# Optimization experiments

Measured on AMD Instinct MI355X. Metric: run time of the kernel, lower is better.

The kernel has to match this reference:

```python
import math
import jax, jax.numpy as jnp
from jax import lax
import numpy as np

N_IMG = 2
C = 128
IMG_H, IMG_W = 512, 1024
STRIDES = (4, 8, 16, 32, 64)
SIZES = (32.0, 64.0, 128.0, 256.0, 512.0)
RATIOS = (0.5, 1.0, 2.0)
A = len(RATIOS)
PRE_NMS_TOPK = 2000    # pre_nms_topk[self.training] with training=True
POST_NMS_TOPK = 1000   # post_nms_topk[self.training]
NMS_THRESH = 0.7
BATCH_PER_IMG = 256
POS_FRAC = 0.5
MIN_BOX_SIZE = 0.0
SCALE_CLAMP = math.log(1000.0 / 16.0)
MATCH_LOW, MATCH_HIGH = 0.3, 0.7


def cell_anchors(size):
    rs = jnp.asarray(RATIOS, jnp.float32)
    area = size * size
    w = jnp.sqrt(area / rs)
    h = w * rs
    return jnp.stack([-w / 2, -h / 2, w / 2, h / 2], axis=1)  # [A,4]


def level_anchors(H, W, stride, size):
    ca = cell_anchors(size)
    sx = jnp.arange(W, dtype=jnp.float32) * stride
    sy = jnp.arange(H, dtype=jnp.float32) * stride
    yy, xx = jnp.meshgrid(sy, sx, indexing="ij")
    shifts = jnp.stack([xx, yy, xx, yy], axis=-1).reshape(-1, 4)  # [H*W,4]
    return (shifts[:, None, :] + ca[None, :, :]).reshape(-1, 4)  # [H*W*A,4]


def pairwise_iou(a, b):
    lt = jnp.maximum(a[:, None, :2], b[None, :, :2])
    rb = jnp.minimum(a[:, None, 2:], b[None, :, 2:])
    wh = jnp.clip(rb - lt, 0.0)
    inter = wh[..., 0] * wh[..., 1]
    area_a = (a[:, 2] - a[:, 0]) * (a[:, 3] - a[:, 1])
    area_b = (b[:, 2] - b[:, 0]) * (b[:, 3] - b[:, 1])
    union = area_a[:, None] + area_b[None, :] - inter
    return jnp.where(inter > 0, inter / union, 0.0)


def get_deltas(src, tgt):
    sw = src[..., 2] - src[..., 0]; sh = src[..., 3] - src[..., 1]
    scx = src[..., 0] + 0.5 * sw;   scy = src[..., 1] + 0.5 * sh
    tw = tgt[..., 2] - tgt[..., 0]; th = tgt[..., 3] - tgt[..., 1]
    tcx = tgt[..., 0] + 0.5 * tw;   tcy = tgt[..., 1] + 0.5 * th
    return jnp.stack([(tcx - scx) / sw, (tcy - scy) / sh,
                      jnp.log(tw / sw), jnp.log(th / sh)], axis=-1)


def apply_deltas(deltas, boxes):
    w = boxes[..., 2] - boxes[..., 0]; h = boxes[..., 3] - boxes[..., 1]
    cx = boxes[..., 0] + 0.5 * w;      cy = boxes[..., 1] + 0.5 * h
    dx, dy = deltas[..., 0], deltas[..., 1]
    dw = jnp.minimum(deltas[..., 2], SCALE_CLAMP)
    dh = jnp.minimum(deltas[..., 3], SCALE_CLAMP)
    pcx = dx * w + cx; pcy = dy * h + cy
    pw = jnp.exp(dw) * w; ph = jnp.exp(dh) * h
    return jnp.stack([pcx - 0.5 * pw, pcy - 0.5 * ph,
                      pcx + 0.5 * pw, pcy + 0.5 * ph], axis=-1)


def conv(x, w, b):
    y = lax.conv_general_dilated(x, w, (1, 1), "SAME",
                                 dimension_numbers=("NCHW", "OIHW", "NCHW"))
    return y + b[None, :, None, None]


def rpn_forward_flat(feats, conv_w, conv_b, obj_w, obj_b, delta_w, delta_b):
    anchors, logits, deltas = [], [], []
    for (stride, size), f in zip(zip(STRIDES, SIZES), feats):
        N, _, H, W = f.shape
        h = jax.nn.relu(conv(f, conv_w, conv_b))
        lg = conv(h, obj_w, obj_b)       # [N,A,H,W]
        dl = conv(h, delta_w, delta_b)   # [N,4A,H,W]
        logits.append(lg.transpose(0, 2, 3, 1).reshape(N, -1))                     # [N,HWA]
        deltas.append(dl.reshape(N, A, 4, H, W).transpose(0, 3, 4, 1, 2).reshape(N, -1, 4))
        anchors.append(level_anchors(H, W, stride, size))
    return anchors, logits, deltas


def label_and_sample(gt_b, key, anchors_all):
    iou = pairwise_iou(gt_b, anchors_all)                 # [G,R]
    matched_idxs = jnp.argmax(iou, axis=0)
    matched_vals = jnp.max(iou, axis=0)
    labels = jnp.where(matched_vals >= MATCH_HIGH, 1,
             jnp.where(matched_vals >= MATCH_LOW, -1, 0))
    highest = jnp.max(iou, axis=1)                        # per-gt best IoU
    lq = jnp.any((iou == highest[:, None]) & (highest[:, None] > 0), axis=0)
    labels = jnp.where(lq, 1, labels)                     # allow_low_quality_matches
    R = labels.shape[0]
    kf, kb = jax.random.split(key)
    fg = labels == 1; bg = labels == 0
    num_fg = jnp.minimum(fg.sum(), int(POS_FRAC * BATCH_PER_IMG))
    num_bg = jnp.minimum(bg.sum(), BATCH_PER_IMG - num_fg)
    def pick(mask, k, num):
        pri = jnp.where(mask, jax.random.uniform(k, (R,)), jnp.inf)
        rank = jnp.argsort(jnp.argsort(pri))
        return rank < num
    sel_fg = pick(fg, kf, num_fg)
    sel_bg = pick(bg, kb, num_bg)
    labels = jnp.where(sel_fg, 1, jnp.where(sel_bg, 0, -1))
    return labels, gt_b[matched_idxs]


def losses_fn(anchors_all, logits_cat, deltas_cat, gt_labels, matched_gt):
    fg = (gt_labels == 1).astype(logits_cat.dtype)          # [N,R]
    gt_deltas = get_deltas(anchors_all[None], matched_gt)   # [N,R,4]
    loc = jnp.sum(jnp.abs(deltas_cat - gt_deltas) * fg[..., None])  # smooth_l1, beta=0
    valid = (gt_labels >= 0).astype(logits_cat.dtype)
    x = logits_cat
    bce = jnp.maximum(x, 0.0) - x * fg + jnp.log1p(jnp.exp(-jnp.abs(x)))
    cls = jnp.sum(bce * valid)
    norm = float(BATCH_PER_IMG) * logits_cat.shape[0]
    return jnp.stack([cls / norm, loc / norm])


def nms_keep(boxes, valid):
    # boxes are sorted by descending score; greedy suppression.
    K = boxes.shape[0]
    iou = pairwise_iou(boxes, boxes)
    idx = jnp.arange(K)
    def body(i, keep):
        sup = (iou[i] > NMS_THRESH) & (idx > i) & keep[i]
        return keep & ~sup
    return lax.fori_loop(0, K, body, valid)


def predict_proposals(anchors, logits, deltas):
    lvl_boxes, lvl_scores = [], []
    for anc, lg, dl in zip(anchors, logits, deltas):
        boxes = apply_deltas(dl, anc[None])             # [N,R_l,4]
        k = min(PRE_NMS_TOPK, lg.shape[1])
        ts, ti = lax.top_k(lg, k)                       # [N,k]
        tb = jnp.take_along_axis(boxes, ti[..., None], axis=1)
        tb = jnp.stack([jnp.clip(tb[..., 0], 0.0, IMG_W), jnp.clip(tb[..., 1], 0.0, IMG_H),
                        jnp.clip(tb[..., 2], 0.0, IMG_W), jnp.clip(tb[..., 3], 0.0, IMG_H)], -1)
        valid = ((tb[..., 2] - tb[..., 0]) > MIN_BOX_SIZE) & ((tb[..., 3] - tb[..., 1]) > MIN_BOX_SIZE)
        keep = jax.vmap(nms_keep)(tb, valid)
        lvl_boxes.append(tb)
        lvl_scores.append(jnp.where(keep, ts, -jnp.inf))
    all_b = jnp.concatenate(lvl_boxes, axis=1)
    all_s = jnp.concatenate(lvl_scores, axis=1)
    fs, fi = lax.top_k(all_s, POST_NMS_TOPK)
    fb = jnp.take_along_axis(all_b, fi[..., None], axis=1)
    return fb, fs


def setup_inputs() -> dict:
    key = jax.random.key(0)
    ks = jax.random.split(key, 12)
    out = {}
    for i, s in enumerate(STRIDES):
        out[f"feat_p{i+2}"] = jax.random.normal(ks[i], (N_IMG, C, IMG_H // s, IMG_W // s), jnp.float32)
    G = 32
    wh_scale = jnp.asarray([IMG_W, IMG_H], jnp.float32)
    cxy = jax.random.uniform(ks[5], (N_IMG, G, 2)) * wh_scale
    wh = 32.0 + jax.random.uniform(ks[6], (N_IMG, G, 2)) * 224.0
    x1y1 = jnp.clip(cxy - wh / 2, 0.0)
    x2y2 = jnp.maximum(jnp.minimum(cxy + wh / 2, wh_scale), x1y1 + 1.0)
    out["gt_boxes"] = jnp.concatenate([x1y1, x2y2], axis=-1)
    out["conv_w"] = 0.01 * jax.random.normal(ks[7], (C, C, 3, 3), jnp.float32)
    out["conv_b"] = jnp.zeros((C,), jnp.float32)
    out["obj_w"] = 0.01 * jax.random.normal(ks[8], (A, C, 1, 1), jnp.float32)
    out["obj_b"] = jnp.zeros((A,), jnp.float32)
    out["delta_w"] = 0.01 * jax.random.normal(ks[9], (4 * A, C, 1, 1), jnp.float32)
    out["delta_b"] = jnp.zeros((4 * A,), jnp.float32)
    return out


def reference(feat_p2, feat_p3, feat_p4, feat_p5, feat_p6, gt_boxes,
              conv_w, conv_b, obj_w, obj_b, delta_w, delta_b):
    feats = [feat_p2, feat_p3, feat_p4, feat_p5, feat_p6]
    anchors, logits, deltas = rpn_forward_flat(feats, conv_w, conv_b, obj_w, obj_b, delta_w, delta_b)
    anchors_all = jnp.concatenate(anchors, axis=0)      # [R,4]
    logits_cat = jnp.concatenate(logits, axis=1)        # [N,R]
    deltas_cat = jnp.concatenate(deltas, axis=1)        # [N,R,4]
    keys = jax.random.split(jax.random.key(42), gt_boxes.shape[0])
    gt_labels, matched_gt = jax.vmap(label_and_sample, in_axes=(0, 0, None))(gt_boxes, keys, anchors_all)
    losses = losses_fn(anchors_all, logits_cat, deltas_cat, gt_labels, matched_gt)
    prop_boxes, prop_scores = predict_proposals(
        anchors,
        [lax.stop_gradient(l) for l in logits],
        [lax.stop_gradient(d) for d in deltas])
    return prop_boxes, prop_scores, losses
```

## Files before the change

### kernel.cpp

```cpp
#include <hip/hip_runtime.h>
#include <stdint.h>
#include <math.h>


#define R_TOT   130944
#define HALF_R  65472
#define TOTK    7920
#define SCALE_CLAMP 4.135166556742356

__host__ __device__ inline void threefry(uint32_t k0, uint32_t k1,
                                         uint32_t x0, uint32_t x1,
                                         uint32_t* o0, uint32_t* o1)
{
  uint32_t ks[3]; ks[0]=k0; ks[1]=k1; ks[2]=k0^k1^0x1BD11BDAu;
  x0 += ks[0]; x1 += ks[1];
  const uint32_t rot0[4] = {13u,15u,26u,6u};
  const uint32_t rot1[4] = {17u,29u,16u,24u};
  for (int i = 0; i < 5; i++){
    const uint32_t* rot = (i & 1) ? rot1 : rot0;
    for (int q = 0; q < 4; q++){
      x0 += x1;
      x1 = (x1 << rot[q]) | (x1 >> (32u - rot[q]));
      x1 ^= x0;
    }
    x0 += ks[(i+1)%3];
    x1 += ks[(i+2)%3] + (uint32_t)(i+1);
  }
  *o0 = x0; *o1 = x1;
}

__device__ inline unsigned long long mono64(double v){
  unsigned long long b = (unsigned long long)__double_as_longlong(v);
  return (b & 0x8000000000000000ull) ? ~b : (b | 0x8000000000000000ull);
}

__device__ __forceinline__ double iou_cf(double g0,double g1,double g2,double g3,
                                         double a0,double a1,double a2,double a3){
  #pragma clang fp contract(off)
  double lt0 = fmax(g0,a0), lt1 = fmax(g1,a1);
  double rb0 = fmin(g2,a2), rb1 = fmin(g3,a3);
  double w = rb0-lt0; if (w<0.0) w=0.0;
  double h = rb1-lt1; if (h<0.0) h=0.0;
  double inter = w*h;
  double aa = (g2-g0)*(g3-g1);
  double ab = (a2-a0)*(a3-a1);
  double uni = aa+ab-inter;
  return inter>0.0 ? inter/uni : 0.0;
}

__device__ __forceinline__ void anchor_of(int r, double* o){
  #pragma clang fp contract(off)
  const int    base[5]={0,98304,122880,129024,130560};
  const int    Wl[5]  ={256,128,64,32,16};
  const double strd[5]={4.0,8.0,16.0,32.0,64.0};
  const double size[5]={32.0,64.0,128.0,256.0,512.0};
  const double ratio[3]={0.5,1.0,2.0};
  int l=0; while (l<4 && r>=base[l+1]) l++;
  int rr=r-base[l]; int pix=rr/3; int a=rr-pix*3;
  int x=pix%Wl[l], y=pix/Wl[l];
  double w=sqrt(size[l]*size[l]/ratio[a]);
  double h=w*ratio[a];
  double sx=(double)x*strd[l], sy=(double)y*strd[l];
  o[0]=sx-0.5*w; o[1]=sy-0.5*h; o[2]=sx+0.5*w; o[3]=sy+0.5*h;
}

__device__ inline void bitonic_desc(double* sv, int* si, int M, int tid, int nthr){
  for (int k=2;k<=M;k<<=1)
    for (int j=k>>1;j>0;j>>=1){
      __syncthreads();
      for (int i=tid;i<M;i+=nthr){
        int ixj=i^j;
        if (ixj>i){
          double va=sv[i], vb=sv[ixj]; int ia=si[i], ib=si[ixj];
          bool before = (va>vb) || (va==vb && ia<ib);
          bool up = ((i&k)==0);
          if (up ? !before : before){ sv[i]=vb; sv[ixj]=va; si[i]=ib; si[ixj]=ia; }
        }
      }
    }
  __syncthreads();
}

__device__ inline void bitonic_asc_u(uint32_t* sk, int* si, int M, int tid, int nthr){
  for (int k=2;k<=M;k<<=1)
    for (int j=k>>1;j>0;j>>=1){
      __syncthreads();
      for (int i=tid;i<M;i+=nthr){
        int ixj=i^j;
        if (ixj>i){
          uint32_t ka=sk[i], kb=sk[ixj]; int ia=si[i], ib=si[ixj];
          bool before = (ka<kb) || (ka==kb && ia<ib);
          bool up = ((i&k)==0);
          if (up ? !before : before){ sk[i]=kb; sk[ixj]=ka; si[i]=ib; si[ixj]=ia; }
        }
      }
    }
  __syncthreads();
}

__global__ __launch_bounds__(256) void k_pre(const float* __restrict__ cw,
    float* __restrict__ cwTf, uint32_t* __restrict__ ub,
    uint32_t kf00,uint32_t kf01,uint32_t kb00,uint32_t kb01,
    uint32_t kf10,uint32_t kf11,uint32_t kb10,uint32_t kb11)
{
  const int bx=blockIdx.x, tid=threadIdx.x;
  if (bx < 576){
    int o = bx*256 + tid;
    if (o >= 147456) return;
    int cc = o & 127; int t = o >> 7;
    int k9 = t % 9;  int ci = t / 9;
    cwTf[(size_t)(ci*9+k9)*128 + cc] = cw[(size_t)cc*1152 + ci*9 + k9];
  } else {
    int j = (bx-576)*256 + tid;
    if (j >= 2*R_TOT) return;
    int slot = j / HALF_R; int t = j - slot*HALF_R;
    uint32_t k0,k1;
    if      (slot==0){k0=kf00;k1=kf01;}
    else if (slot==1){k0=kb00;k1=kb01;}
    else if (slot==2){k0=kf10;k1=kf11;}
    else             {k0=kb10;k1=kb11;}
    uint32_t o0,o1;
    threefry(k0,k1,(uint32_t)t,(uint32_t)(t+HALF_R),&o0,&o1);
    ub[(size_t)slot*R_TOT+t]=o0;
    ub[(size_t)slot*R_TOT+t+HALF_R]=o1;
  }
}

#define CTH 4
#define CTW 8

__global__ __launch_bounds__(256,3) void k_conv_all(
    const float* __restrict__ f2, const float* __restrict__ f3,
    const float* __restrict__ f4, const float* __restrict__ f5,
    const float* __restrict__ f6,
    const float* __restrict__ cwTf, const float* __restrict__ cb,
    const float* __restrict__ ow, const float* __restrict__ ob,
    const float* __restrict__ dwt, const float* __restrict__ dbt,
    double* __restrict__ logits, double* __restrict__ dpred)
{
  __shared__ double fshd[4][6][12];
  __shared__ __align__(16) char ush[33792];
  float*  wshF = (float*)ush;
  double* hshp = (double*)ush;
  __shared__ float hw[15*128];
  __shared__ float hb[15];

  const int cumt[6]={0,2048,2560,2688,2720,2728};
  const int Hs[5]={128,64,32,16,8}, Wl[5]={256,128,64,32,16};
  const int rbs[5]={0,98304,122880,129024,130560};
  const int lgx[5]={5,4,3,2,1};

  int bid=blockIdx.x;
  int lvl=0;
  while (lvl<4 && bid>=cumt[lvl+1]) lvl++;
  int t=bid-cumt[lvl];
  const int img=t&1; const int tt=t>>1;
  const int H=Hs[lvl], W=Wl[lvl], rbase=rbs[lvl];
  const int tx=tt&((1<<lgx[lvl])-1), ty=tt>>lgx[lvl];
  const int x0=tx*CTW, y0=ty*CTH;
  const float* f = lvl==0?f2: lvl==1?f3: lvl==2?f4: lvl==3?f5: f6;

  const int tid=threadIdx.x;
  for (int i=tid;i<15*128;i+=256){
    int o=i>>7, c=i&127;
    hw[i]=(o<3)?ow[o*128+c]:dwt[(o-3)*128+c];
  }
  if (tid<15) hb[tid]=(tid<3)?ob[tid]:dbt[tid-3];

  const int c=tid&127, half=tid>>7;
  double acc[16];
  #pragma unroll
  for (int i=0;i<16;i++) acc[i]=0.0;

  const float* fimg = f + (size_t)img*128*H*W;

  const bool fin_act = (tid < 240);
  int ci_f=0,dy_f=0,dx_f=0; bool fin_valid=false;
  const float* fptr=fimg;
  if (fin_act){
    ci_f=tid/60; int rem=tid-ci_f*60; dy_f=rem/10; dx_f=rem-dy_f*10;
    int y=y0-1+dy_f, x=x0-1+dx_f;
    fin_valid = (y>=0&&y<H&&x>=0&&x<W);
    fptr = fimg + (size_t)ci_f*H*W + (fin_valid ? ((size_t)y*W+x) : 0);
  }
  const size_t fstep=(size_t)4*H*W;
  const float2* wsrc=(const float2*)cwTf;

  float fin_pf=0.f; float2 wpf[9];
  if (fin_act){ fin_pf = fin_valid ? *fptr : 0.f; fptr += fstep; }
  #pragma unroll
  for (int j2=0;j2<9;j2++) wpf[j2]=wsrc[tid+j2*256];

  for (int ci0=0; ci0<128; ci0+=4){
    __syncthreads();
    if (fin_act) fshd[ci_f][dy_f][dx_f]=(double)fin_pf;
    { float2* wdst=(float2*)wshF;
      #pragma unroll
      for (int j2=0;j2<9;j2++) wdst[tid+j2*256]=wpf[j2]; }
    if (ci0+4<128){
      if (fin_act){ fin_pf = fin_valid ? *fptr : 0.f; fptr += fstep; }
      const float2* wn = wsrc + (size_t)(ci0+4)*576;
      #pragma unroll
      for (int j2=0;j2<9;j2++) wpf[j2]=wn[tid+j2*256];
    }
    __syncthreads();
    #pragma unroll
    for (int ci=0;ci<4;ci++){
      double w9d[9];
      #pragma unroll
      for (int k=0;k<9;k++) w9d[k]=(double)wshF[(ci*9+k)*128 + c];
      #pragma unroll
      for (int irl=0;irl<4;irl++){
        int ir=half*2+irl;
        double rowb[10];
        #pragma unroll
        for (int q=0;q<10;q++) rowb[q]=fshd[ci][ir][q];
        #pragma unroll
        for (int orl=0;orl<2;orl++){
          int ky=irl-orl;
          if (ky<0||ky>2) continue;
          #pragma unroll
          for (int px=0;px<8;px++){
            double s=acc[orl*8+px];
            #pragma unroll
            for (int kx=0;kx<3;kx++) s += w9d[ky*3+kx]*rowb[px+kx];
            acc[orl*8+px]=s;
          }
        }
      }
    }
  }
  __syncthreads();
  double bc=(double)cb[c];
  #pragma unroll
  for (int pp=0;pp<16;pp++){
    double hv=acc[pp]+bc; if (hv<0.0) hv=0.0;
    hshp[c*33+(half*16+pp)]=hv;
  }
  __syncthreads();
  for (int j=tid;j<480;j+=256){
    int o=j>>5, p=j&31;
    int py=p>>3, px=p&7;
    double s=(double)hb[o];
    for (int c2=0;c2<128;c2++) s += (double)hw[o*128+c2]*hshp[c2*33+p];
    int gy=y0+py, gx=x0+px;
    long long pix=(long long)gy*W+gx;
    size_t rb=(size_t)rbase+(size_t)pix*3;
    if (o<3) logits[(size_t)img*R_TOT+rb+o]=s;
    else { int a=(o-3)>>2, jj=(o-3)&3; dpred[((size_t)img*R_TOT+rb+a)*4+jj]=s; }
  }
}

__global__ __launch_bounds__(256) void k_mid1(const double* __restrict__ dpred,
    double* __restrict__ boxes, const float* __restrict__ gt,
    unsigned long long* __restrict__ highest)
{
  const int bx=blockIdx.x, tid=threadIdx.x;
  if (bx < 1023){
    int idx=bx*256+tid;
    if (idx>=2*R_TOT) return;
    int r = idx<R_TOT ? idx : idx-R_TOT;
    double a[4]; anchor_of(r,a);
    const double* d = dpred + (size_t)idx*4;
    double w=a[2]-a[0], h=a[3]-a[1];
    double cx=a[0]+0.5*w, cy=a[1]+0.5*h;
    double dw=fmin(d[2],SCALE_CLAMP), dh=fmin(d[3],SCALE_CLAMP);
    double pcx=d[0]*w+cx, pcy=d[1]*h+cy;
    double pw=exp(dw)*w, ph=exp(dh)*h;
    double x1=pcx-0.5*pw, y1=pcy-0.5*ph;
    double x2=pcx+0.5*pw, y2=pcy+0.5*ph;
    x1=fmin(fmax(x1,0.0),1024.0); y1=fmin(fmax(y1,0.0),512.0);
    x2=fmin(fmax(x2,0.0),1024.0); y2=fmin(fmax(y2,0.0),512.0);
    double* o=boxes+(size_t)idx*4;
    o[0]=x1; o[1]=y1; o[2]=x2; o[3]=y2;
  } else {
    __shared__ double gts[128];
    __shared__ unsigned long long lmax[32];
    const int gb=bx-1023;
    const int img=gb>>6, b=gb&63;
    if (tid<128) gts[tid]=(double)gt[img*128+tid];
    if (tid<32) lmax[tid]=0ull;
    __syncthreads();
    double gm[32];
    #pragma unroll
    for (int g=0;g<32;g++) gm[g]=0.0;
    for (int r=b*256+tid; r<R_TOT; r+=64*256){
      double a[4]; anchor_of(r,a);
      #pragma unroll
      for (int g=0;g<32;g++){
        double v=iou_cf(gts[g*4],gts[g*4+1],gts[g*4+2],gts[g*4+3],a[0],a[1],a[2],a[3]);
        gm[g]=fmax(gm[g],v);
      }
    }
    #pragma unroll
    for (int g=0;g<32;g++){
      double v=gm[g];
      #pragma unroll
      for (int off=1; off<64; off<<=1) v=fmax(v,__shfl_xor(v,off));
      if ((tid&63)==0) atomicMax(&lmax[g],(unsigned long long)__double_as_longlong(v));
    }
    __syncthreads();
    if (tid<32) atomicMax(&highest[img*32+tid], lmax[tid]);
  }
}

__global__ __launch_bounds__(256) void k_label(const float* __restrict__ gt,
    const unsigned long long* __restrict__ highest,
    int* __restrict__ prelab, int* __restrict__ matched,
    int* __restrict__ labels, int* __restrict__ counts){
  __shared__ double gts[128];
  __shared__ double hg[32];
  __shared__ int wfg[4], wbg[4];
  const int tid=threadIdx.x, img=blockIdx.y;
  if (tid<128) gts[tid]=(double)gt[img*128+tid];
  if (tid<32)  hg[tid]=__longlong_as_double((long long)highest[img*32+tid]);
  __syncthreads();
  int r=blockIdx.x*256+tid;
  const bool ok=(r<R_TOT);
  int lab=-1, bi=0;
  if (ok){
    double a[4]; anchor_of(r,a);
    double best=-1.0; bool lq=false;
    #pragma unroll
    for (int g=0;g<32;g++){
      double v=iou_cf(gts[g*4],gts[g*4+1],gts[g*4+2],gts[g*4+3],a[0],a[1],a[2],a[3]);
      if (v>best){ best=v; bi=g; }
      if (hg[g]>0.0 && v==hg[g]) lq=true;
    }
    lab = lq ? 1 : (best>=0.7 ? 1 : (best>=0.3 ? -1 : 0));
    prelab [(size_t)img*R_TOT+r]=lab;
    matched[(size_t)img*R_TOT+r]=bi;
    labels [(size_t)img*R_TOT+r]=-1;
  }
  unsigned long long bf=__ballot(ok && lab==1);
  unsigned long long bb=__ballot(ok && lab==0);
  const int wid=tid>>6, lane=tid&63;
  if (lane==0){ wfg[wid]=__popcll(bf); wbg[wid]=__popcll(bb); }
  __syncthreads();
  if (tid==0){
    int fcnt=wfg[0]+wfg[1]+wfg[2]+wfg[3];
    int bcnt=wbg[0]+wbg[1]+wbg[2]+wbg[3];
    if (fcnt) atomicAdd(&counts[img*2+0],fcnt);
    if (bcnt) atomicAdd(&counts[img*2+1],bcnt);
  }
}

__global__ __launch_bounds__(1024) void k_mid2(const uint32_t* __restrict__ ub,
    const int* __restrict__ prelab, const int* __restrict__ counts,
    int* __restrict__ labels,
    const double* __restrict__ logits, const double* __restrict__ boxes,
    double* __restrict__ allS, double* __restrict__ allB)
{
  __shared__ __align__(16) char buf[49152];
  __shared__ int hist[256];
  __shared__ int sI0, sI1; __shared__ unsigned long long sT;
  __shared__ int cnt;
  const int tid=threadIdx.x;

  if (blockIdx.x < 4){
    uint32_t* skey=(uint32_t*)buf; int* sidx=(int*)(buf+16384);
    const int img=blockIdx.x>>1, cls=blockIdx.x&1;
    const int cfg=counts[img*2+0], cbg=counts[img*2+1];
    const int num_fg=cfg<128?cfg:128;
    const int cap_bg=256-num_fg;
    const int num=cls?(cbg<cap_bg?cbg:cap_bg):num_fg;
    if (num<=0) return;
    const int want=cls?0:1;
    const int sel=want;
    const uint32_t* u=ub+(size_t)(img*2+cls)*R_TOT;
    const int* pl=prelab+(size_t)img*R_TOT;
    int* lab=labels+(size_t)img*R_TOT;

    for (int b=tid;b<256;b+=1024) hist[b]=0;
    if (tid==0) cnt=0;
    __syncthreads();
    for (int r=tid;r<R_TOT;r+=1024){
      int plr = pl[r];
      uint32_t key = u[r]>>9;
      if (plr==want) atomicAdd(&hist[key>>15],1);
    }
    __syncthreads();
    if (tid==0){
      int cum=0,b=0;
      for (;b<255;b++){ int hh=hist[b]; if (cum+hh>=num) break; cum+=hh; }
      sI0=b; sI1=num-cum;
    }
    __syncthreads();
    const uint32_t bsel=(uint32_t)sI0; const int kneed=sI1;
    for (int r=tid;r<R_TOT;r+=1024){
      int plr = pl[r];
      uint32_t key = u[r]>>9;
      if (plr==want){
        uint32_t t8=key>>15;
        if (t8<bsel) lab[r]=sel;
        else if (t8==bsel){ int p=atomicAdd(&cnt,1); if (p<4096){ skey[p]=key; sidx[p]=r; } }
      }
    }
    __syncthreads();
    int n=cnt<4096?cnt:4096;
    for (int i=tid;i<4096;i+=1024) if (i>=n){ skey[i]=0xFFFFFFFFu; sidx[i]=0x7FFFFFFF; }
    bitonic_asc_u(skey,sidx,4096,tid,1024);
    int take = kneed<n?kneed:n;
    for (int i=tid;i<take;i+=1024) lab[sidx[i]]=sel;
  } else {
    double* sv=(double*)buf; int* si=(int*)(buf+32768);
    const int Rl[5]   ={98304,24576,6144,1536,384};
    const int kl[5]   ={2000,2000,2000,1536,384};
    const int lbase[5]={0,98304,122880,129024,130560};
    const int loff[5] ={0,2000,4000,6000,7536};
    const int bb=blockIdx.x-4;
    const int lvl=bb%5, img=bb/5;
    const int Rn=Rl[lvl], K=kl[lvl];
    const double* lg=logits+(size_t)img*R_TOT+lbase[lvl];

    unsigned long long chosen=0; int kneed=K;
    for (int ps=7; ps>=6; --ps){
      int shift=ps*8;
      for (int b=tid;b<256;b+=1024) hist[b]=0;
      __syncthreads();
      for (int r=tid;r<Rn;r+=1024){
        unsigned long long ik=~mono64(lg[r]);
        bool okp=(ps==7)||((ik>>(shift+8))==(chosen>>(shift+8)));
        if (okp) atomicAdd(&hist[(int)((ik>>shift)&255)],1);
      }
      __syncthreads();
      if (tid==0){
        int cum=0,b=0;
        for (;b<255;b++){ int hh=hist[b]; if (cum+hh>=kneed) break; cum+=hh; }
        sT=chosen|((unsigned long long)b<<shift); sI1=kneed-cum;
      }
      __syncthreads();
      chosen=sT; kneed=sI1;
      __syncthreads();
    }
    const unsigned long long lim = chosen | 0xFFFFFFFFFFFFull;
    if (tid==0) cnt=0;
    __syncthreads();
    for (int r=tid;r<Rn;r+=1024){
      unsigned long long ik=~mono64(lg[r]);
      if (ik<=lim){ int p=atomicAdd(&cnt,1); if (p<4096){ sv[p]=lg[r]; si[p]=r; } }
    }
    __syncthreads();
    int n=cnt<4096?cnt:4096;
    for (int i=tid;i<4096;i+=1024) if (i>=n){ sv[i]=-HUGE_VAL; si[i]=0x7FFFFFFF; }
    bitonic_desc(sv,si,4096,tid,1024);
    for (int j=tid;j<K;j+=1024){
      double v=sv[j]; int r=si[j];
      size_t slot=(size_t)img*TOTK+loff[lvl]+j;
      allS[slot]=v;
      const double* bx=boxes+((size_t)img*R_TOT+lbase[lvl]+r)*4;
      allB[slot*4+0]=bx[0]; allB[slot*4+1]=bx[1]; allB[slot*4+2]=bx[2]; allB[slot*4+3]=bx[3];
    }
  }
}

__global__ __launch_bounds__(256) void k_mid3(const double* __restrict__ allB,
    unsigned long long* __restrict__ msk,
    const double* __restrict__ logits, const double* __restrict__ dpred,
    const float* __restrict__ gt, const int* __restrict__ labels,
    const int* __restrict__ matched, double* __restrict__ part)
{
  const int bx=blockIdx.x, tid=threadIdx.x;
  if (bx < 1980){
    __shared__ double Bsh[8000];
    const int kl[5]  ={2000,2000,2000,1536,384};
    const int loff[5]={0,2000,4000,6000,7536};
    const int rbc[6] ={0,250,500,750,942,990};
    const int img = bx/990; int t = bx - img*990;
    int lvl=0; while (lvl<4 && t>=rbc[lvl+1]) lvl++;
    const int i0=(t-rbc[lvl])*8;
    const int K=kl[lvl]; const int nw=(K+63)>>6;
    const double* B=allB+(size_t)(img*TOTK+loff[lvl])*4;
    for (int q=tid;q<K*4;q+=256) Bsh[q]=B[q];
    __syncthreads();
    const int wv=tid>>6, lane=tid&63;
    for (int rr=0;rr<8;rr++){
      int i=i0+rr;
      if (i>=K) break;
      const double bi0=Bsh[i*4],bi1=Bsh[i*4+1],bi2=Bsh[i*4+2],bi3=Bsh[i*4+3];
      const double areai=(bi2-bi0)*(bi3-bi1);
      for (int w=wv;w<nw;w+=4){
        int j=w*64+lane;
        bool pred=false;
        if (j<K && j>i){
          double a0=Bsh[j*4],a1=Bsh[j*4+1],a2=Bsh[j*4+2],a3=Bsh[j*4+3];
          double lt0=fmax(bi0,a0), lt1=fmax(bi1,a1);
          double rb0=fmin(bi2,a2), rb1=fmin(bi3,a3);
          double ww=rb0-lt0; if (ww<0.0) ww=0.0;
          double hh=rb1-lt1; if (hh<0.0) hh=0.0;
          double inter=ww*hh;
          double uni=areai+(a2-a0)*(a3-a1)-inter;
          double iou=inter>0.0?inter/uni:0.0;
          pred = iou>0.7;
        }
        unsigned long long m=__ballot(pred);
        if (lane==0) msk[((size_t)img*TOTK+loff[lvl]+i)*32+w]=m;
      }
    }
  } else {
    const int bid2=bx-1980;
    double cls=0.0, loc=0.0;
    for (int idx=bid2*256+tid; idx<2*R_TOT; idx+=256*256){
      int l=labels[idx];
      if (l<0) continue;
      double x=logits[idx];
      double fgv=(l==1)?1.0:0.0;
      cls += fmax(x,0.0)-x*fgv+log1p(exp(-fabs(x)));
      if (l==1){
        int img=idx/R_TOT, r=idx-img*R_TOT;
        double a[4]; anchor_of(r,a);
        int m=matched[idx];
        const float* g=gt+img*128+m*4;
        double sw=a[2]-a[0], sh=a[3]-a[1];
        double scx=a[0]+0.5*sw, scy=a[1]+0.5*sh;
        double tw=(double)g[2]-(double)g[0], th=(double)g[3]-(double)g[1];
        double tcx=(double)g[0]+0.5*tw, tcy=(double)g[1]+0.5*th;
        double d0=(tcx-scx)/sw, d1=(tcy-scy)/sh;
        double d2=log(tw/sw), d3=log(th/sh);
        const double* dp=dpred+(size_t)idx*4;
        loc += fabs(dp[0]-d0)+fabs(dp[1]-d1)+fabs(dp[2]-d2)+fabs(dp[3]-d3);
      }
    }
    __shared__ double sc[256], sl[256];
    sc[tid]=cls; sl[tid]=loc; __syncthreads();
    for (int s=128;s>0;s>>=1){
      if (tid<s){ sc[tid]+=sc[tid+s]; sl[tid]+=sl[tid+s]; }
      __syncthreads();
    }
    if (tid==0){ part[bid2*2]=sc[0]; part[bid2*2+1]=sl[0]; }
  }
}

#define NMS_LD(BUF, BASE) do{ \
  _Pragma("unroll") \
  for (int j_=0;j_<16;j_++){ int i_=(BASE)+j_; \
    BUF[j_] = (lane<nw && i_<K) ? M[(size_t)i_*32+lane] : 0ull; } \
}while(0)
#define NMS_PR(BUF, BASE) do{ \
  _Pragma("unroll") \
  for (int j_=0;j_<16;j_++){ int i_=(BASE)+j_; \
    if (i_<K){ unsigned long long kw_=__shfl(keep,(i_>>6)); \
      if ((kw_>>(i_&63))&1ull) keep &= ~BUF[j_]; } } \
}while(0)

__global__ void k_nmsscan(const double* __restrict__ allB, double* __restrict__ allS,
    const unsigned long long* __restrict__ msk){
  const int kl[5]  ={2000,2000,2000,1536,384};
  const int loff[5]={0,2000,4000,6000,7536};
  const int lvl=blockIdx.x, img=blockIdx.y;
  const int K=kl[lvl], off=loff[lvl], nw=(K+63)>>6;
  const int lane=threadIdx.x;
  const double* B=allB+(size_t)(img*TOTK+off)*4;
  const unsigned long long* M=msk+((size_t)img*TOTK+off)*32;
  unsigned long long keep=0ull;
  if (lane<nw){
    for (int b=0;b<64;b++){
      int j=lane*64+b;
      if (j<K){
        double x1=B[(size_t)j*4],y1=B[(size_t)j*4+1],x2=B[(size_t)j*4+2],y2=B[(size_t)j*4+3];
        if ((x2-x1)>0.0 && (y2-y1)>0.0) keep|=(1ull<<b);
      }
    }
  }
  unsigned long long Abuf[16], Bbuf[16];
  NMS_LD(Abuf, 0);
  for (int base=0; base<K; base+=32){
    NMS_LD(Bbuf, base+16);
    NMS_PR(Abuf, base);
    NMS_LD(Abuf, base+32);
    NMS_PR(Bbuf, base+16);
  }
  if (lane<nw){
    for (int b=0;b<64;b++){
      int j=lane*64+b;
      if (j<K && !((keep>>b)&1ull))
        allS[(size_t)img*TOTK+off+j]=-HUGE_VAL;
    }
  }
}

__global__ __launch_bounds__(1024) void k_final(const double* __restrict__ allS,
    const double* __restrict__ allB, const double* __restrict__ part,
    float* __restrict__ out){
  const int tid=threadIdx.x;
  if (blockIdx.x==2){
    __shared__ double sc[256], sl[256];
    if (tid<256){ sc[tid]=part[tid*2]; sl[tid]=part[tid*2+1]; }
    __syncthreads();
    for (int s=128;s>0;s>>=1){
      if (tid<s){ sc[tid]+=sc[tid+s]; sl[tid]+=sl[tid+s]; }
      __syncthreads();
    }
    if (tid==0){ out[10000]=(float)(sc[0]/512.0); out[10001]=(float)(sl[0]/512.0); }
    return;
  }
  const int img=blockIdx.x;
  const double* sarr=allS+(size_t)img*TOTK;
  __shared__ int hist[256];
  __shared__ unsigned long long sT; __shared__ int sK;
  __shared__ double sv[4096]; __shared__ int si[4096]; __shared__ int cnt;

  unsigned long long chosen=0; int kneed=1000;
  for (int ps=7; ps>=0; --ps){
    int shift=ps*8;
    for (int b=tid;b<256;b+=1024) hist[b]=0;
    __syncthreads();
    for (int r=tid;r<TOTK;r+=1024){
      unsigned long long ik=~mono64(sarr[r]);
      bool okp=(ps==7)||((ik>>(shift+8))==(chosen>>(shift+8)));
      if (okp) atomicAdd(&hist[(int)((ik>>shift)&255)],1);
    }
    __syncthreads();
    if (tid==0){
      int cum=0,b=0;
      for (;b<255;b++){ int hh=hist[b]; if (cum+hh>=kneed) break; cum+=hh; }
      sT=chosen|((unsigned long long)b<<shift); sK=kneed-cum;
    }
    __syncthreads();
    chosen=sT; kneed=sK;
    __syncthreads();
  }
  if (tid==0) cnt=0;
  __syncthreads();
  for (int r=tid;r<TOTK;r+=1024){
    unsigned long long ik=~mono64(sarr[r]);
    if (ik<=chosen){ int p=atomicAdd(&cnt,1); if (p<4096){ sv[p]=sarr[r]; si[p]=r; } }
  }
  __syncthreads();
  int n=cnt<4096?cnt:4096;
  for (int i=tid;i<4096;i+=1024) if (i>=n){ sv[i]=-HUGE_VAL; si[i]=0x7FFFFFFF; }
  bitonic_desc(sv,si,4096,tid,1024);
  for (int j=tid;j<1000;j+=1024){
    out[8000+img*1000+j]=(float)sv[j];
    int idx=si[j];
    const double* b=allB+((size_t)img*TOTK+idx)*4;
    float* ob=out+((size_t)img*1000+j)*4;
    ob[0]=(float)b[0]; ob[1]=(float)b[1]; ob[2]=(float)b[2]; ob[3]=(float)b[3];
  }
}

extern "C" void kernel_launch(void* const* d_in, const int* in_sizes, int n_in,
                              void* d_out, int out_size, void* d_ws, size_t ws_size,
                              hipStream_t stream)
{
  (void)in_sizes; (void)n_in; (void)out_size;
  const float* feats[5];
  for (int i=0;i<5;i++) feats[i]=(const float*)d_in[i];
  const float* gt =(const float*)d_in[5];
  const float* cw =(const float*)d_in[6];
  const float* cb =(const float*)d_in[7];
  const float* ow =(const float*)d_in[8];
  const float* ob =(const float*)d_in[9];
  const float* dwt=(const float*)d_in[10];
  const float* dbt=(const float*)d_in[11];
  float* out=(float*)d_out;

  char* p=(char*)d_ws;
  auto carve=[&](size_t nbytes)->char*{ char* q=p; p += (nbytes+255)&~(size_t)255; return q; };
  double* logits =(double*)carve(2ull*R_TOT*8);
  double* dpred  =(double*)carve(2ull*R_TOT*4*8);
  double* boxes  =(double*)carve(2ull*R_TOT*4*8);
  float* cwTf    =(float*)carve(147456ull*4);
  uint32_t* ub   =(uint32_t*)carve(4ull*R_TOT*4);
  int* prelab    =(int*)carve(2ull*R_TOT*4);
  int* matched   =(int*)carve(2ull*R_TOT*4);
  int* labels    =(int*)carve(2ull*R_TOT*4);
  unsigned long long* highest=(unsigned long long*)carve(2*32*8);
  int* counts    =(int*)carve(256);
  double* allS   =(double*)carve(2ull*TOTK*8);
  double* allB   =(double*)carve(2ull*TOTK*4*8);
  unsigned long long* msk=(unsigned long long*)carve(2ull*TOTK*32*8);
  double* part   =(double*)carve(256*2*8);
  if ((size_t)(p-(char*)d_ws) > ws_size) return;

  hipMemsetAsync(highest, 0, 768, stream);

  uint32_t a0,b0,a1,b1;
  threefry(0u,42u,0u,2u,&a0,&b0);
  threefry(0u,42u,1u,3u,&a1,&b1);
  uint32_t kf00,kf01,kb00,kb01,kf10,kf11,kb10,kb11;
  { uint32_t c0,d0,c1,d1;
    threefry(a0,a1,0u,2u,&c0,&d0); threefry(a0,a1,1u,3u,&c1,&d1);
    kf00=c0; kf01=c1; kb00=d0; kb01=d1;
    threefry(b0,b1,0u,2u,&c0,&d0); threefry(b0,b1,1u,3u,&c1,&d1);
    kf10=c0; kf11=c1; kb10=d0; kb11=d1; }

  k_pre<<<1599, 256, 0, stream>>>(cw, cwTf, ub, kf00,kf01,kb00,kb01,kf10,kf11,kb10,kb11);
  k_conv_all<<<2728, 256, 0, stream>>>(feats[0],feats[1],feats[2],feats[3],feats[4],
                                       cwTf,cb,ow,ob,dwt,dbt, logits, dpred);
  k_mid1<<<1151, 256, 0, stream>>>(dpred, boxes, gt, highest);
  k_label<<<dim3(512,2), 256, 0, stream>>>(gt, highest, prelab, matched, labels, counts);
  k_mid2<<<14, 1024, 0, stream>>>(ub, prelab, counts, labels, logits, boxes, allS, allB);
  k_mid3<<<2236, 256, 0, stream>>>(allB, msk, logits, dpred, gt, labels, matched, part);
  k_nmsscan<<<dim3(5,2), 64, 0, stream>>>(allB, allS, msk);
  k_final<<<3, 1024, 0, stream>>>(allS, allB, part, out);
}
```

Measured before the change: 1.445 ms.

## Fuse IoU max and labeling into existing kernels; decode boxes lazily for top-K

The per-GT highest-IoU reduction moves into the preprocessing kernel, and anchor labeling is appended as extra blocks of the conv kernel, so it runs alongside the convolution tiles. The full box decode pass over all anchors is removed; boxes are decoded only for the selected top-K candidates inside k_mid2. This cuts two launches and a large intermediate buffer write and read. The cost is more blocks in the conv launch and decode work added to the serial top-K stage.

```diff
diff --git a/kernel.cpp b/kernel.cpp
--- a/kernel.cpp
+++ b/kernel.cpp
@@ -64,6 +64,20 @@
   o[0]=sx-0.5*w; o[1]=sy-0.5*h; o[2]=sx+0.5*w; o[3]=sy+0.5*h;
 }
 
+__device__ __forceinline__ void decode_box(int ridx, const double* __restrict__ d,
+                                           double* __restrict__ o){
+  double a[4]; anchor_of(ridx,a);
+  double w=a[2]-a[0], h=a[3]-a[1];
+  double cx=a[0]+0.5*w, cy=a[1]+0.5*h;
+  double dw=fmin(d[2],SCALE_CLAMP), dh=fmin(d[3],SCALE_CLAMP);
+  double pcx=d[0]*w+cx, pcy=d[1]*h+cy;
+  double pw=exp(dw)*w, ph=exp(dh)*h;
+  double x1=pcx-0.5*pw, y1=pcy-0.5*ph;
+  double x2=pcx+0.5*pw, y2=pcy+0.5*ph;
+  o[0]=fmin(fmax(x1,0.0),1024.0); o[1]=fmin(fmax(y1,0.0),512.0);
+  o[2]=fmin(fmax(x2,0.0),1024.0); o[3]=fmin(fmax(y2,0.0),512.0);
+}
+
 __device__ inline void bitonic_desc(double* sv, int* si, int M, int tid, int nthr){
   for (int k=2;k<=M;k<<=1)
     for (int j=k>>1;j>0;j>>=1){
@@ -100,6 +114,7 @@
 
 __global__ __launch_bounds__(256) void k_pre(const float* __restrict__ cw,
     float* __restrict__ cwTf, uint32_t* __restrict__ ub,
+    const float* __restrict__ gt, unsigned long long* __restrict__ highest,
     uint32_t kf00,uint32_t kf01,uint32_t kb00,uint32_t kb01,
     uint32_t kf10,uint32_t kf11,uint32_t kb10,uint32_t kb11)
 {
@@ -110,7 +125,7 @@
     int cc = o & 127; int t = o >> 7;
     int k9 = t % 9;  int ci = t / 9;
     cwTf[(size_t)(ci*9+k9)*128 + cc] = cw[(size_t)cc*1152 + ci*9 + k9];
-  } else {
+  } else if (bx < 1599){
     int j = (bx-576)*256 + tid;
     if (j >= 2*R_TOT) return;
     int slot = j / HALF_R; int t = j - slot*HALF_R;
@@ -123,20 +138,51 @@
     threefry(k0,k1,(uint32_t)t,(uint32_t)(t+HALF_R),&o0,&o1);
     ub[(size_t)slot*R_TOT+t]=o0;
     ub[(size_t)slot*R_TOT+t+HALF_R]=o1;
+  } else {
+    __shared__ double gts[128];
+    __shared__ unsigned long long lmax[32];
+    const int gb=bx-1599;
+    const int img=gb>>6, b=gb&63;
+    if (tid<128) gts[tid]=(double)gt[img*128+tid];
+    if (tid<32) lmax[tid]=0ull;
+    __syncthreads();
+    double gm[32];
+    #pragma unroll
+    for (int g=0;g<32;g++) gm[g]=0.0;
+    for (int r=b*256+tid; r<R_TOT; r+=64*256){
+      double a[4]; anchor_of(r,a);
+      #pragma unroll
+      for (int g=0;g<32;g++){
+        double v=iou_cf(gts[g*4],gts[g*4+1],gts[g*4+2],gts[g*4+3],a[0],a[1],a[2],a[3]);
+        gm[g]=fmax(gm[g],v);
+      }
+    }
+    #pragma unroll
+    for (int g=0;g<32;g++){
+      double v=gm[g];
+      #pragma unroll
+      for (int off=1; off<64; off<<=1) v=fmax(v,__shfl_xor(v,off));
+      if ((tid&63)==0) atomicMax(&lmax[g],(unsigned long long)__double_as_longlong(v));
+    }
+    __syncthreads();
+    if (tid<32) atomicMax(&highest[img*32+tid], lmax[tid]);
   }
 }
 
 #define CTH 4
 #define CTW 8
 
-__global__ __launch_bounds__(256,3) void k_conv_all(
+__global__ __launch_bounds__(256,3) void k_conv_label(
     const float* __restrict__ f2, const float* __restrict__ f3,
     const float* __restrict__ f4, const float* __restrict__ f5,
     const float* __restrict__ f6,
     const float* __restrict__ cwTf, const float* __restrict__ cb,
     const float* __restrict__ ow, const float* __restrict__ ob,
     const float* __restrict__ dwt, const float* __restrict__ dbt,
-    double* __restrict__ logits, double* __restrict__ dpred)
+    double* __restrict__ logits, double* __restrict__ dpred,
+    const float* __restrict__ gt, const unsigned long long* __restrict__ highest,
+    int* __restrict__ prelab, int* __restrict__ matched,
+    int* __restrict__ labels, int* __restrict__ counts)
 {
   __shared__ double fshd[4][6][12];
   __shared__ __align__(16) char ush[33792];
@@ -144,6 +190,48 @@
   double* hshp = (double*)ush;
   __shared__ float hw[15*128];
   __shared__ float hb[15];
+
+  const int tid=threadIdx.x;
+
+  if (blockIdx.x >= 2728){
+    double* gts=(double*)ush;
+    double* hg =(double*)(ush+1024);
+    int* wfg=(int*)(ush+1280); int* wbg=(int*)(ush+1296);
+    const int lb=blockIdx.x-2728;
+    const int img=lb>>9, blk=lb&511;
+    if (tid<128) gts[tid]=(double)gt[img*128+tid];
+    if (tid<32)  hg[tid]=__longlong_as_double((long long)highest[img*32+tid]);
+    __syncthreads();
+    int r=blk*256+tid;
+    const bool ok=(r<R_TOT);
+    int lab=-1, bi=0;
+    if (ok){
+      double a[4]; anchor_of(r,a);
+      double best=-1.0; bool lq=false;
+      #pragma unroll
+      for (int g=0;g<32;g++){
+        double v=iou_cf(gts[g*4],gts[g*4+1],gts[g*4+2],gts[g*4+3],a[0],a[1],a[2],a[3]);
+        if (v>best){ best=v; bi=g; }
+        if (hg[g]>0.0 && v==hg[g]) lq=true;
+      }
+      lab = lq ? 1 : (best>=0.7 ? 1 : (best>=0.3 ? -1 : 0));
+      prelab [(size_t)img*R_TOT+r]=lab;
+      matched[(size_t)img*R_TOT+r]=bi;
+      labels [(size_t)img*R_TOT+r]=-1;
+    }
+    unsigned long long bf=__ballot(ok && lab==1);
+    unsigned long long bb=__ballot(ok && lab==0);
+    const int wid=tid>>6, lane=tid&63;
+    if (lane==0){ wfg[wid]=__popcll(bf); wbg[wid]=__popcll(bb); }
+    __syncthreads();
+    if (tid==0){
+      int fcnt=wfg[0]+wfg[1]+wfg[2]+wfg[3];
+      int bcnt=wbg[0]+wbg[1]+wbg[2]+wbg[3];
+      if (fcnt) atomicAdd(&counts[img*2+0],fcnt);
+      if (bcnt) atomicAdd(&counts[img*2+1],bcnt);
+    }
+    return;
+  }
 
   const int cumt[6]={0,2048,2560,2688,2720,2728};
   const int Hs[5]={128,64,32,16,8}, Wl[5]={256,128,64,32,16};
@@ -160,7 +248,6 @@
   const int x0=tx*CTW, y0=ty*CTH;
   const float* f = lvl==0?f2: lvl==1?f3: lvl==2?f4: lvl==3?f5: f6;
 
-  const int tid=threadIdx.x;
   for (int i=tid;i<15*128;i+=256){
     int o=i>>7, c=i&127;
     hw[i]=(o<3)?ow[o*128+c]:dwt[(o-3)*128+c];
@@ -251,104 +338,10 @@
   }
 }
 
-__global__ __launch_bounds__(256) void k_mid1(const double* __restrict__ dpred,
-    double* __restrict__ boxes, const float* __restrict__ gt,
-    unsigned long long* __restrict__ highest)
-{
-  const int bx=blockIdx.x, tid=threadIdx.x;
-  if (bx < 1023){
-    int idx=bx*256+tid;
-    if (idx>=2*R_TOT) return;
-    int r = idx<R_TOT ? idx : idx-R_TOT;
-    double a[4]; anchor_of(r,a);
-    const double* d = dpred + (size_t)idx*4;
-    double w=a[2]-a[0], h=a[3]-a[1];
-    double cx=a[0]+0.5*w, cy=a[1]+0.5*h;
-    double dw=fmin(d[2],SCALE_CLAMP), dh=fmin(d[3],SCALE_CLAMP);
-    double pcx=d[0]*w+cx, pcy=d[1]*h+cy;
-    double pw=exp(dw)*w, ph=exp(dh)*h;
-    double x1=pcx-0.5*pw, y1=pcy-0.5*ph;
-    double x2=pcx+0.5*pw, y2=pcy+0.5*ph;
-    x1=fmin(fmax(x1,0.0),1024.0); y1=fmin(fmax(y1,0.0),512.0);
-    x2=fmin(fmax(x2,0.0),1024.0); y2=fmin(fmax(y2,0.0),512.0);
-    double* o=boxes+(size_t)idx*4;
-    o[0]=x1; o[1]=y1; o[2]=x2; o[3]=y2;
-  } else {
-    __shared__ double gts[128];
-    __shared__ unsigned long long lmax[32];
-    const int gb=bx-1023;
-    const int img=gb>>6, b=gb&63;
-    if (tid<128) gts[tid]=(double)gt[img*128+tid];
-    if (tid<32) lmax[tid]=0ull;
-    __syncthreads();
-    double gm[32];
-    #pragma unroll
-    for (int g=0;g<32;g++) gm[g]=0.0;
-    for (int r=b*256+tid; r<R_TOT; r+=64*256){
-      double a[4]; anchor_of(r,a);
-      #pragma unroll
-      for (int g=0;g<32;g++){
-        double v=iou_cf(gts[g*4],gts[g*4+1],gts[g*4+2],gts[g*4+3],a[0],a[1],a[2],a[3]);
-        gm[g]=fmax(gm[g],v);
-      }
-    }
-    #pragma unroll
-    for (int g=0;g<32;g++){
-      double v=gm[g];
-      #pragma unroll
-      for (int off=1; off<64; off<<=1) v=fmax(v,__shfl_xor(v,off));
-      if ((tid&63)==0) atomicMax(&lmax[g],(unsigned long long)__double_as_longlong(v));
-    }
-    __syncthreads();
-    if (tid<32) atomicMax(&highest[img*32+tid], lmax[tid]);
-  }
-}
-
-__global__ __launch_bounds__(256) void k_label(const float* __restrict__ gt,
-    const unsigned long long* __restrict__ highest,
-    int* __restrict__ prelab, int* __restrict__ matched,
-    int* __restrict__ labels, int* __restrict__ counts){
-  __shared__ double gts[128];
-  __shared__ double hg[32];
-  __shared__ int wfg[4], wbg[4];
-  const int tid=threadIdx.x, img=blockIdx.y;
-  if (tid<128) gts[tid]=(double)gt[img*128+tid];
-  if (tid<32)  hg[tid]=__longlong_as_double((long long)highest[img*32+tid]);
-  __syncthreads();
-  int r=blockIdx.x*256+tid;
-  const bool ok=(r<R_TOT);
-  int lab=-1, bi=0;
-  if (ok){
-    double a[4]; anchor_of(r,a);
-    double best=-1.0; bool lq=false;
-    #pragma unroll
-    for (int g=0;g<32;g++){
-      double v=iou_cf(gts[g*4],gts[g*4+1],gts[g*4+2],gts[g*4+3],a[0],a[1],a[2],a[3]);
-      if (v>best){ best=v; bi=g; }
-      if (hg[g]>0.0 && v==hg[g]) lq=true;
-    }
-    lab = lq ? 1 : (best>=0.7 ? 1 : (best>=0.3 ? -1 : 0));
-    prelab [(size_t)img*R_TOT+r]=lab;
-    matched[(size_t)img*R_TOT+r]=bi;
-    labels [(size_t)img*R_TOT+r]=-1;
-  }
-  unsigned long long bf=__ballot(ok && lab==1);
-  unsigned long long bb=__ballot(ok && lab==0);
-  const int wid=tid>>6, lane=tid&63;
-  if (lane==0){ wfg[wid]=__popcll(bf); wbg[wid]=__popcll(bb); }
-  __syncthreads();
-  if (tid==0){
-    int fcnt=wfg[0]+wfg[1]+wfg[2]+wfg[3];
-    int bcnt=wbg[0]+wbg[1]+wbg[2]+wbg[3];
-    if (fcnt) atomicAdd(&counts[img*2+0],fcnt);
-    if (bcnt) atomicAdd(&counts[img*2+1],bcnt);
-  }
-}
-
 __global__ __launch_bounds__(1024) void k_mid2(const uint32_t* __restrict__ ub,
     const int* __restrict__ prelab, const int* __restrict__ counts,
     int* __restrict__ labels,
-    const double* __restrict__ logits, const double* __restrict__ boxes,
+    const double* __restrict__ logits, const double* __restrict__ dpred,
     double* __restrict__ allS, double* __restrict__ allB)
 {
   __shared__ __align__(16) char buf[49152];
@@ -448,7 +441,9 @@
       double v=sv[j]; int r=si[j];
       size_t slot=(size_t)img*TOTK+loff[lvl]+j;
       allS[slot]=v;
-      const double* bx=boxes+((size_t)img*R_TOT+lbase[lvl]+r)*4;
+      int ridx=lbase[lvl]+r;
+      double bx[4];
+      decode_box(ridx, dpred+((size_t)img*R_TOT+ridx)*4, bx);
       allB[slot*4+0]=bx[0]; allB[slot*4+1]=bx[1]; allB[slot*4+2]=bx[2]; allB[slot*4+3]=bx[3];
     }
   }
@@ -659,7 +654,6 @@
   auto carve=[&](size_t nbytes)->char*{ char* q=p; p += (nbytes+255)&~(size_t)255; return q; };
   double* logits =(double*)carve(2ull*R_TOT*8);
   double* dpred  =(double*)carve(2ull*R_TOT*4*8);
-  double* boxes  =(double*)carve(2ull*R_TOT*4*8);
   float* cwTf    =(float*)carve(147456ull*4);
   uint32_t* ub   =(uint32_t*)carve(4ull*R_TOT*4);
   int* prelab    =(int*)carve(2ull*R_TOT*4);
@@ -685,12 +679,12 @@
     threefry(b0,b1,0u,2u,&c0,&d0); threefry(b0,b1,1u,3u,&c1,&d1);
     kf10=c0; kf11=c1; kb10=d0; kb11=d1; }
 
-  k_pre<<<1599, 256, 0, stream>>>(cw, cwTf, ub, kf00,kf01,kb00,kb01,kf10,kf11,kb10,kb11);
-  k_conv_all<<<2728, 256, 0, stream>>>(feats[0],feats[1],feats[2],feats[3],feats[4],
-                                       cwTf,cb,ow,ob,dwt,dbt, logits, dpred);
-  k_mid1<<<1151, 256, 0, stream>>>(dpred, boxes, gt, highest);
-  k_label<<<dim3(512,2), 256, 0, stream>>>(gt, highest, prelab, matched, labels, counts);
-  k_mid2<<<14, 1024, 0, stream>>>(ub, prelab, counts, labels, logits, boxes, allS, allB);
+  k_pre<<<1727, 256, 0, stream>>>(cw, cwTf, ub, gt, highest,
+      kf00,kf01,kb00,kb01,kf10,kf11,kb10,kb11);
+  k_conv_label<<<3752, 256, 0, stream>>>(feats[0],feats[1],feats[2],feats[3],feats[4],
+      cwTf,cb,ow,ob,dwt,dbt, logits, dpred,
+      gt, highest, prelab, matched, labels, counts);
+  k_mid2<<<14, 1024, 0, stream>>>(ub, prelab, counts, labels, logits, dpred, allS, allB);
   k_mid3<<<2236, 256, 0, stream>>>(allB, msk, logits, dpred, gt, labels, matched, part);
   k_nmsscan<<<dim3(5,2), 64, 0, stream>>>(allB, allS, msk);
   k_final<<<3, 1024, 0, stream>>>(allS, allB, part, out);
```

New measurement: 1.424 ms. Within noise of the previous version (-1.5%).
